# Kernel optimization log

Measured on AMD Instinct MI355X. Metric: run time of the kernel, lower is better.

The kernel has to match this reference:

```python
import jax, jax.numpy as jnp
import numpy as np

DIM = 256
HEADS = 8
HEAD_DIM = DIM // HEADS
WS = 7            # window size
SHIFT = 3         # shift size
H = 56
W = 56
B = 32
WA = WS * WS      # window area = 49
NWH, NWW = H // WS, W // WS
NW = NWH * NWW    # windows per image


def _make_attn_mask():
    # replicate the torch mask construction for the shifted windows
    img = np.zeros((H, W), dtype=np.float32)
    cnt = 0
    for hs in (slice(0, -WS), slice(-WS, -SHIFT), slice(-SHIFT, None)):
        for ws_ in (slice(0, -WS), slice(-WS, -SHIFT), slice(-SHIFT, None)):
            img[hs, ws_] = cnt
            cnt += 1
    mw = img.reshape(NWH, WS, NWW, WS).transpose(0, 2, 1, 3).reshape(-1, WA)  # (nW, 49)
    diff = mw[:, None, :] - mw[:, :, None]                                    # (nW, 49, 49)
    return np.where(diff != 0, -100.0, 0.0).astype(np.float32)


def _make_rel_index():
    coords = np.stack(np.meshgrid(np.arange(WS), np.arange(WS), indexing='ij')).reshape(2, -1)
    rel = coords[:, :, None] - coords[:, None, :]        # (2, 49, 49)
    rel = rel.transpose(1, 2, 0) + (WS - 1)              # shift to >= 0
    rel[..., 0] *= 2 * WS - 1
    return rel.sum(-1).astype(np.int32)                  # (49, 49) in [0, 169)


def setup_inputs() -> dict:
    key = jax.random.key(0)
    ks = jax.random.split(key, 12)
    s = 0.02
    inp = {
        'x': jax.random.normal(ks[0], (B, H, W, DIM), dtype=jnp.float32),
        'ln1_w': jnp.ones((DIM,), jnp.float32), 'ln1_b': jnp.zeros((DIM,), jnp.float32),
        'qkv_w': s * jax.random.normal(ks[1], (3 * DIM, DIM), jnp.float32),
        'qkv_b': jnp.zeros((3 * DIM,), jnp.float32),
        'rpb_table': s * jax.random.normal(ks[2], ((2 * WS - 1) ** 2, HEADS), jnp.float32),
        'proj_w': s * jax.random.normal(ks[3], (DIM, DIM), jnp.float32),
        'proj_b': jnp.zeros((DIM,), jnp.float32),
        'ln2_w': jnp.ones((DIM,), jnp.float32), 'ln2_b': jnp.zeros((DIM,), jnp.float32),
        'fc1_w': s * jax.random.normal(ks[4], (4 * DIM, DIM), jnp.float32),
        'fc1_b': jnp.zeros((4 * DIM,), jnp.float32),
        'ln3_w': jnp.ones((4 * DIM,), jnp.float32), 'ln3_b': jnp.zeros((4 * DIM,), jnp.float32),
        'fc2_w': s * jax.random.normal(ks[5], (DIM, 4 * DIM), jnp.float32),
        'fc2_b': jnp.zeros((DIM,), jnp.float32),
        'attn_mask': jnp.asarray(_make_attn_mask()),     # (nW, 49, 49)
        'rel_index': jnp.asarray(_make_rel_index()),     # (49, 49) int32
    }
    return inp


def _ln(x, w, b, eps=1e-5):
    m = jnp.mean(x, axis=-1, keepdims=True)
    v = jnp.mean((x - m) ** 2, axis=-1, keepdims=True)
    return (x - m) * jax.lax.rsqrt(v + eps) * w + b


def reference(x, ln1_w, ln1_b, qkv_w, qkv_b, rpb_table, proj_w, proj_b,
              ln2_w, ln2_b, fc1_w, fc1_b, ln3_w, ln3_b, fc2_w, fc2_b,
              attn_mask, rel_index):
    Bn, Hn, Wn, C = x.shape
    # ---- attention branch ----
    y = _ln(x, ln1_w, ln1_b)
    sh = jnp.roll(y, (-SHIFT, -SHIFT), axis=(1, 2))
    # window partition: (B, H, W, C) -> (B*nW, 49, C)
    win = sh.reshape(Bn, NWH, WS, NWW, WS, C).transpose(0, 1, 3, 2, 4, 5).reshape(Bn * NW, WA, C)
    qkv = win @ qkv_w.T + qkv_b                              # (Bw, 49, 3C)
    qkv = qkv.reshape(Bn * NW, WA, 3, HEADS, HEAD_DIM).transpose(2, 0, 3, 1, 4)
    q, k, v = qkv[0], qkv[1], qkv[2]                         # (Bw, h, 49, d)
    scale = HEAD_DIM ** -0.5
    attn = jnp.einsum('bhqd,bhkd->bhqk', q * scale, k)       # (Bw, h, 49, 49)
    bias = rpb_table[rel_index]                              # (49, 49, h)
    attn = attn + jnp.transpose(bias, (2, 0, 1))[None]
    attn = attn.reshape(Bn, NW, HEADS, WA, WA) + attn_mask[None, :, None]
    attn = jax.nn.softmax(attn, axis=-1).reshape(Bn * NW, HEADS, WA, WA)
    out = jnp.einsum('bhqk,bhkd->bhqd', attn, v)             # (Bw, h, 49, d)
    out = out.transpose(0, 2, 1, 3).reshape(Bn * NW, WA, C)
    out = out @ proj_w.T + proj_b
    # window reverse + un-shift
    out = out.reshape(Bn, NWH, NWW, WS, WS, C).transpose(0, 1, 3, 2, 4, 5).reshape(Bn, Hn, Wn, C)
    out = jnp.roll(out, (SHIFT, SHIFT), axis=(1, 2))
    x = x + out
    # ---- MLP branch (note: extra LayerNorm inside MLP per source) ----
    z = _ln(x, ln2_w, ln2_b)
    h = jax.nn.gelu(z @ fc1_w.T + fc1_b, approximate=False)
    h = _ln(h, ln3_w, ln3_b)
    x = x + (h @ fc2_w.T + fc2_b)
    return x
```

## Files before the change

### kernel.cpp

```cpp
#include <hip/hip_runtime.h>
#include <hip/hip_bf16.h>
#include <math.h>

typedef __attribute__((ext_vector_type(8))) short bf16x8;
typedef __attribute__((ext_vector_type(4))) float f32x4;
typedef __attribute__((ext_vector_type(4))) float f4;
typedef __attribute__((ext_vector_type(8))) unsigned short us8;
typedef __attribute__((ext_vector_type(4))) unsigned short us4;
typedef unsigned short u16;
typedef unsigned int u32;

#define HEADS 8
#define SHIFT_ 3
#define HIMG 56
#define WIMG 56
#define WA 49
#define NTOK 100352
#define NPAIR 16384

static __device__ __forceinline__ float bf2f(u16 v){ return __uint_as_float(((u32)v)<<16); }
static __device__ __forceinline__ u16 f2bf(float f){
  u32 u = __float_as_uint(f);
  return (u16)((u + 0x7fffu + ((u>>16)&1u)) >> 16);
}
static __device__ __forceinline__ u32 pkbf(float a, float b){
  __hip_bfloat162 h = __float22bfloat162_rn(make_float2(a, b));
  return *reinterpret_cast<u32*>(&h);
}
static __device__ __forceinline__ float wsum(float v){
  #pragma unroll
  for (int off=32; off>0; off>>=1) v += __shfl_xor(v, off, 64);
  return v;
}
static __device__ __forceinline__ void glds16(const u16* g, u16* l){
  __builtin_amdgcn_global_load_lds(
      (const __attribute__((address_space(1))) unsigned int*)g,
      (__attribute__((address_space(3))) unsigned int*)l, 16, 0, 0);
}
static __device__ __forceinline__ int tok2pix(int row){
  int bw = row / 49, t = row - bw*49;
  int b  = bw >> 6,  w = bw & 63;
  int wh = w >> 3,   ww = w & 7;
  int th = t / 7,    tw = t - th*7;
  int r = wh*7 + th + SHIFT_; if (r >= HIMG) r -= HIMG;
  int c = ww*7 + tw + SHIFT_; if (c >= WIMG) c -= WIMG;
  return (b*HIMG + r)*WIMG + c;
}
static __device__ __forceinline__ float gelu_f(float x){
  float e = __expf(-1.702f*x);
  return x*__builtin_amdgcn_rcpf(1.0f+e);
}

template<int C, int ISBF>
__global__ void ln_stats_kernel(const void* __restrict__ srcv, float* __restrict__ stats){
  int wave = threadIdx.x >> 6, lane = threadIdx.x & 63;
  int tok = blockIdx.x*4 + wave;
  float s=0.f, s2=0.f;
  if (ISBF == 0){
    const float* p = (const float*)srcv + (size_t)tok*C;
    #pragma unroll
    for (int i=0;i<C/256;i++){
      f4 v = *(const f4*)(p + lane*4*(C/256) + i*4);
      #pragma unroll
      for (int e=0;e<4;e++){ float f=v[e]; s+=f; s2+=f*f; }
    }
  } else {
    const u16* p = (const u16*)srcv + (size_t)tok*C;
    #pragma unroll
    for (int i=0;i<C/512;i++){
      us8 v = *(const us8*)(p + lane*8*(C/512) + i*8);
      #pragma unroll
      for (int e=0;e<8;e++){ float f=bf2f(v[e]); s+=f; s2+=f*f; }
    }
  }
  s = wsum(s); s2 = wsum(s2);
  if (lane==0){
    float mean = s/(float)C;
    float var  = s2/(float)C - mean*mean;
    stats[2*tok]   = mean;
    stats[2*tok+1] = rsqrtf(var + 1e-5f);
  }
}

__global__ void ln_apply_kernel(const float* __restrict__ src, u16* __restrict__ dst){
  int wave = threadIdx.x >> 6, lane = threadIdx.x & 63;
  int tok = blockIdx.x*4 + wave;
  const float* p = src + (size_t)tok*256;
  f4 a = *(const f4*)(p + lane*4);
  float s = a[0]+a[1]+a[2]+a[3];
  float s2 = a[0]*a[0]+a[1]*a[1]+a[2]*a[2]+a[3]*a[3];
  s = wsum(s); s2 = wsum(s2);
  float mean = s*(1.f/256.f);
  float var  = s2*(1.f/256.f) - mean*mean;
  float rstd = rsqrtf(var + 1e-5f);
  u32 o2[2];
  o2[0] = pkbf((a[0]-mean)*rstd, (a[1]-mean)*rstd);
  o2[1] = pkbf((a[2]-mean)*rstd, (a[3]-mean)*rstd);
  *(u32*)(dst + (size_t)tok*256 + lane*4)     = o2[0];
  *(u32*)(dst + (size_t)tok*256 + lane*4 + 2) = o2[1];
}

__global__ void ln_apply_b_kernel(const u16* __restrict__ src, u16* __restrict__ dst,
                                  float* __restrict__ st){
  int wave = threadIdx.x >> 6, lane = threadIdx.x & 63;
  int tok = blockIdx.x*4 + wave;
  const u16* p = src + (size_t)tok*256 + lane*4;
  us4 a4 = *(const us4*)p;
  float a0=bf2f(a4[0]), a1=bf2f(a4[1]), a2=bf2f(a4[2]), a3=bf2f(a4[3]);
  float s = a0+a1+a2+a3;
  float s2 = a0*a0+a1*a1+a2*a2+a3*a3;
  s = wsum(s); s2 = wsum(s2);
  float mean = s*(1.f/256.f);
  float var  = s2*(1.f/256.f) - mean*mean;
  float rstd = rsqrtf(var + 1e-5f);
  u32 o0 = pkbf((a0-mean)*rstd, (a1-mean)*rstd);
  u32 o1 = pkbf((a2-mean)*rstd, (a3-mean)*rstd);
  u16* d = dst + (size_t)tok*256 + lane*4;
  *(u32*)d     = o0;
  *(u32*)(d+2) = o1;
  if (lane==0){ st[2*tok] = mean; st[2*tok+1] = rstd; }
}

__global__ void prep_weights(
    const float* __restrict__ qkv_w, const float* __restrict__ qkv_b,
    const float* __restrict__ ln1w,  const float* __restrict__ ln1b,
    const float* __restrict__ fc1_w, const float* __restrict__ fc1_b,
    const float* __restrict__ ln2w,  const float* __restrict__ ln2b,
    const float* __restrict__ fc2_w, const float* __restrict__ fc2_b,
    const float* __restrict__ ln3w,  const float* __restrict__ ln3b,
    const float* __restrict__ proj_w, const float* __restrict__ proj_b,
    u16* __restrict__ wq, float* __restrict__ bq,
    u16* __restrict__ w1, float* __restrict__ b1,
    u16* __restrict__ w2, float* __restrict__ b2,
    u16* __restrict__ wp, float* __restrict__ bp,
    float* __restrict__ cs2, float* __restrict__ hstats)
{
  for (int idx = blockIdx.x*256 + threadIdx.x; idx < 2*NTOK; idx += gridDim.x*256)
    hstats[idx] = 0.f;

  int wave = threadIdx.x>>6, lane = threadIdx.x&63;
  int n = blockIdx.x*4 + wave;
  const float *W,*lw,*lb,*bs; u16* WO; float* BO; int K, row, noln, docs;
  float qs = 1.f;
  if (n < 768)      { W=qkv_w; lw=ln1w; lb=ln1b; bs=qkv_b; WO=wq; BO=bq; K=256;  row=n;      noln=0; docs=0;
                      if (n < 256) qs = 0.17677669529663689f; }
  else if (n < 1792){ W=fc1_w; lw=ln2w; lb=ln2b; bs=fc1_b; WO=w1; BO=b1; K=256;  row=n-768;  noln=0; docs=0; }
  else if (n < 2048){ W=fc2_w; lw=ln3w; lb=ln3b; bs=fc2_b; WO=w2; BO=b2; K=1024; row=n-1792; noln=0; docs=1; }
  else              { W=proj_w; lw=nullptr; lb=nullptr; bs=proj_b; WO=wp; BO=bp; K=256; row=n-2048; noln=1; docs=0; }
  float dot = 0.f, cs = 0.f;
  for (int k=lane; k<K; k+=64){
    float wv = W[(size_t)row*K + k];
    if (noln){
      WO[(size_t)row*K + k] = f2bf(wv);
    } else {
      dot += wv * lb[k];
      u16 q = f2bf(wv * lw[k] * qs);
      WO[(size_t)row*K + k] = q;
      cs += bf2f(q);
    }
  }
  dot = wsum(dot);
  if (docs){ cs = wsum(cs); if (lane==0) cs2[row] = cs; }
  if (lane==0) BO[row] = (bs[row] + dot) * qs;
}

template<int SMODE, int EPI, int SWAP, int DEPTH>
__global__ __launch_bounds__(256)
void gemm18(const void* __restrict__ Av, const u16* __restrict__ Bt,
            const float* __restrict__ stats, float* __restrict__ hstats,
            const float* __restrict__ biasf, const float* __restrict__ resid,
            const float* __restrict__ colsum, void* __restrict__ outv,
            int K, int NT, int CHUNK)
{
  constexpr int BM=128, BN=128, BK=32;
  constexpr int NBUF = DEPTH + 1;
  __shared__ u16 smem[NBUF*8192];
  constexpr int BOFF = NBUF*4096;
  int b = blockIdx.x;
  int linear = (b & 7)*CHUNK + (b >> 3);
  int mt = linear / NT, nt = linear - mt*NT;
  int m0 = mt*BM, n0 = nt*BN;
  int tid  = threadIdx.x;
  int lane = tid & 63, wave = tid >> 6;
  int wr = wave >> 1, wc = wave & 1;
  int lc16 = lane & 15, g = lane >> 4;
  int nsteps = K >> 5;

  const u16* asrc[2];
  const u16* bsrc[2];
  #pragma unroll
  for (int i=0;i<2;i++){
    int c = tid + i*256;
    int row = c >> 2, gch = ((c & 3) - (row >> 1)) & 3;
    if (SMODE <= 1){
      int grow = (SMODE==0) ? tok2pix(m0+row) : (m0+row);
      asrc[i] = (const u16*)Av + (size_t)grow*K + gch*8;
    }
    bsrc[i] = Bt + (size_t)(n0+row)*K + gch*8;
  }
  float smean[2], srstd[2];
  if (SMODE == 3){
    #pragma unroll
    for (int i=0;i<2;i++){
      int grow = m0 + ((tid + i*256) >> 2);
      smean[i] = stats[2*grow]; srstd[i] = stats[2*grow+1];
    }
  }

  f32x4 acc[4][4];
  #pragma unroll
  for (int i=0;i<4;i++)
    #pragma unroll
    for (int j=0;j<4;j++){ acc[i][j][0]=0.f; acc[i][j][1]=0.f; acc[i][j][2]=0.f; acc[i][j][3]=0.f; }

  if (SMODE <= 1){
    #pragma unroll
    for (int pt=0; pt<DEPTH; ++pt){
      int kt = pt << 5;
      #pragma unroll
      for (int i=0;i<2;i++) glds16(asrc[i]+kt, smem + pt*4096 + i*2048 + wave*512);
      #pragma unroll
      for (int i=0;i<2;i++) glds16(bsrc[i]+kt, smem + BOFF + pt*4096 + i*2048 + wave*512);
    }
    if (DEPTH == 3)      asm volatile("s_waitcnt vmcnt(8)" ::: "memory");
    else                 asm volatile("s_waitcnt vmcnt(4)" ::: "memory");
    __builtin_amdgcn_s_barrier();

    int cur = 0;
    for (int t=0; t<nsteps; ++t){
      if (t+DEPTH < nsteps){
        int ktD = (t+DEPTH) << 5;
        int nb = cur + DEPTH; if (nb >= NBUF) nb -= NBUF;
        int off = nb*4096;
        #pragma unroll
        for (int i=0;i<2;i++) glds16(asrc[i]+ktD, smem + off + i*2048 + wave*512);
        #pragma unroll
        for (int i=0;i<2;i++) glds16(bsrc[i]+ktD, smem + BOFF + off + i*2048 + wave*512);
      }
      const u16* Ap = smem + cur*4096;
      const u16* Bp = smem + BOFF + cur*4096;
      bf16x8 af[4], bfr[4];
      #pragma unroll
      for (int mi=0;mi<4;mi++){
        int r = wr*64 + mi*16 + lc16;
        u32 byte = (u32)(r*64) + ((u32)((g + (r>>1)) & 3) << 4);
        af[mi] = *(const bf16x8*)(Ap + (byte>>1));
      }
      #pragma unroll
      for (int ni=0;ni<4;ni++){
        int r = wc*64 + ni*16 + lc16;
        u32 byte = (u32)(r*64) + ((u32)((g + (r>>1)) & 3) << 4);
        bfr[ni] = *(const bf16x8*)(Bp + (byte>>1));
      }
      #pragma unroll
      for (int mi=0;mi<4;mi++)
        #pragma unroll
        for (int ni=0;ni<4;ni++)
          acc[mi][ni] = SWAP ? __builtin_amdgcn_mfma_f32_16x16x32_bf16(bfr[ni], af[mi], acc[mi][ni], 0, 0, 0)
                             : __builtin_amdgcn_mfma_f32_16x16x32_bf16(af[mi], bfr[ni], acc[mi][ni], 0, 0, 0);
      int rem = nsteps - 1 - t;
      int cnt = (rem < DEPTH) ? rem : DEPTH;
      if (cnt >= 3)      asm volatile("s_waitcnt vmcnt(8)" ::: "memory");
      else if (cnt == 2) asm volatile("s_waitcnt vmcnt(4)" ::: "memory");
      else if (cnt == 1) asm volatile("s_waitcnt vmcnt(0)" ::: "memory");
      __builtin_amdgcn_s_barrier();
      cur = (cur+1 == NBUF) ? 0 : cur+1;
    }
  } else {
    f4 rcurf[2][2];
    #pragma unroll
    for (int i=0;i<2;i++){
      int c = tid + i*256; int row = c>>2, gch = ((c&3) - (row>>1)) & 3;
      const float* ap = (const float*)Av + (size_t)(m0+row)*K + gch*8;
      rcurf[i][0] = *(const f4*)ap; rcurf[i][1] = *(const f4*)(ap+4);
    }
    for (int t=0; t<nsteps; ++t){
      int kt = t << 5;
      #pragma unroll
      for (int i=0;i<2;i++){
        int c = tid + i*256; int row = c>>2, s = c&3;
        us8 o;
        #pragma unroll
        for (int e=0;e<8;e++){
          float fv = rcurf[i][e>>2][e&3];
          o[e] = f2bf((fv - smean[i])*srstd[i]);
        }
        u32 byte = (u32)(row*64) + ((u32)s << 4);
        *(us8*)(smem + (byte>>1)) = o;
      }
      #pragma unroll
      for (int i=0;i<2;i++) glds16(bsrc[i]+kt, smem + BOFF + i*2048 + wave*512);
      __syncthreads();
      if (t+1 < nsteps){
        int kt1 = kt + 32;
        #pragma unroll
        for (int i=0;i<2;i++){
          int c = tid + i*256; int row = c>>2, gch = ((c&3) - (row>>1)) & 3;
          const float* ap = (const float*)Av + (size_t)(m0+row)*K + kt1 + gch*8;
          rcurf[i][0] = *(const f4*)ap; rcurf[i][1] = *(const f4*)(ap+4);
        }
      }
      bf16x8 af[4], bfr[4];
      #pragma unroll
      for (int mi=0;mi<4;mi++){
        int r = wr*64 + mi*16 + lc16;
        u32 byte = (u32)(r*64) + ((u32)((g + (r>>1)) & 3) << 4);
        af[mi] = *(const bf16x8*)(smem + (byte>>1));
      }
      #pragma unroll
      for (int ni=0;ni<4;ni++){
        int r = wc*64 + ni*16 + lc16;
        u32 byte = (u32)(r*64) + ((u32)((g + (r>>1)) & 3) << 4);
        bfr[ni] = *(const bf16x8*)(smem + BOFF + (byte>>1));
      }
      #pragma unroll
      for (int mi=0;mi<4;mi++)
        #pragma unroll
        for (int ni=0;ni<4;ni++)
          acc[mi][ni] = SWAP ? __builtin_amdgcn_mfma_f32_16x16x32_bf16(bfr[ni], af[mi], acc[mi][ni], 0, 0, 0)
                             : __builtin_amdgcn_mfma_f32_16x16x32_bf16(af[mi], bfr[ni], acc[mi][ni], 0, 0, 0);
      __syncthreads();
    }
  }

  int lr = lane >> 4;
  if (EPI==0){
    u16* Cs = smem;
    #pragma unroll
    for (int mi=0;mi<4;mi++){
      #pragma unroll
      for (int ni=0;ni<4;ni++){
        int cl = wc*64 + ni*16 + lc16;
        float bv = biasf[n0 + cl];
        #pragma unroll
        for (int j=0;j<4;j++){
          int rl = wr*64 + mi*16 + lr*4 + j;
          float v = acc[mi][ni][j] + bv;
          u32 byte = (u32)(rl*256 + cl*2) ^ ((u32)(rl&7)<<4);
          Cs[byte>>1] = f2bf(v);
        }
      }
    }
    __syncthreads();
    #pragma unroll
    for (int i=0;i<8;i++){
      int c = tid + i*256;
      int rl = c>>4, c0 = (c&15)*8;
      u32 byte = (u32)(rl*256 + c0*2) ^ ((u32)(rl&7)<<4);
      us8 v = *(const us8*)(Cs + (byte>>1));
      int row = m0 + rl, col = n0 + c0;
      int which = col>>8, hh = (col>>5)&7, d0 = col&31;
      int bwi = row/49, t = row - bwi*49;
      *(us8*)((u16*)outv + ((size_t)which*NPAIR + bwi*8 + hh)*(WA*32) + t*32 + d0) = v;
    }
  } else if (EPI==2){
    u16* Cs = smem;
    #pragma unroll
    for (int mi=0;mi<4;mi++){
      int rl = wr*64 + mi*16 + lc16;
      float ss = 0.f, sq = 0.f;
      #pragma unroll
      for (int ni=0;ni<4;ni++){
        int cl = wc*64 + ni*16 + g*4;
        f4 bv = *(const f4*)(biasf + n0 + cl);
        float v0 = gelu_f(acc[mi][ni][0] + bv[0]);
        float v1 = gelu_f(acc[mi][ni][1] + bv[1]);
        float v2 = gelu_f(acc[mi][ni][2] + bv[2]);
        float v3 = gelu_f(acc[mi][ni][3] + bv[3]);
        ss += (v0+v1)+(v2+v3);
        sq += (v0*v0+v1*v1)+(v2*v2+v3*v3);
        u32 w0 = pkbf(v0, v1), w1 = pkbf(v2, v3);
        u32 byte = (u32)(rl*256 + cl*2) ^ ((u32)(rl&7)<<4);
        *(u32*)(Cs + (byte>>1))     = w0;
        *(u32*)(Cs + (byte>>1) + 2) = w1;
      }
      ss += __shfl_xor(ss, 16, 64); ss += __shfl_xor(ss, 32, 64);
      sq += __shfl_xor(sq, 16, 64); sq += __shfl_xor(sq, 32, 64);
      if (g==0){
        int grow = m0 + rl;
        atomicAdd(&hstats[2*grow],   ss);
        atomicAdd(&hstats[2*grow+1], sq);
      }
    }
    __syncthreads();
    #pragma unroll
    for (int i=0;i<8;i++){
      int c = tid + i*256;
      int rl = c>>4, c0 = (c&15)*8;
      u32 byte = (u32)(rl*256 + c0*2) ^ ((u32)(rl&7)<<4);
      us8 v = *(const us8*)(Cs + (byte>>1));
      int row = m0 + rl, col = n0 + c0;
      *(us8*)((u16*)outv + (size_t)row*1024 + col) = v;
    }
  } else if (EPI==5){
    u16* Cs = smem;
    #pragma unroll
    for (int mi=0;mi<4;mi++){
      int rl = wr*64 + mi*16 + lc16;
      int pix = tok2pix(m0 + rl);
      #pragma unroll
      for (int ni=0;ni<4;ni++){
        int cl = wc*64 + ni*16 + g*4;
        int col = n0 + cl;
        f4 bv = *(const f4*)(biasf + col);
        f4 rr = *(const f4*)(resid + (size_t)pix*256 + col);
        float v0 = acc[mi][ni][0] + bv[0] + rr[0];
        float v1 = acc[mi][ni][1] + bv[1] + rr[1];
        float v2 = acc[mi][ni][2] + bv[2] + rr[2];
        float v3 = acc[mi][ni][3] + bv[3] + rr[3];
        u32 w0 = pkbf(v0, v1), w1 = pkbf(v2, v3);
        u32 byte = (u32)(rl*256 + cl*2) ^ ((u32)(rl&7)<<4);
        *(u32*)(Cs + (byte>>1))     = w0;
        *(u32*)(Cs + (byte>>1) + 2) = w1;
      }
    }
    __syncthreads();
    #pragma unroll
    for (int i=0;i<8;i++){
      int c = tid + i*256;
      int rl = c>>4, c0 = (c&15)*8;
      u32 byte = (u32)(rl*256 + c0*2) ^ ((u32)(rl&7)<<4);
      us8 v = *(const us8*)(Cs + (byte>>1));
      int pix = tok2pix(m0 + rl);
      *(us8*)((u16*)outv + (size_t)pix*256 + n0 + c0) = v;
    }
  } else {
    #pragma unroll
    for (int mi=0;mi<4;mi++){
      int rl = wr*64 + mi*16 + lc16;
      int grow = m0 + rl;
      float rs = 1.f, mr = 0.f, istd2 = 0.f, mean2 = 0.f;
      if (EPI==4 || EPI==6){
        float s = stats[2*grow], q = stats[2*grow+1];
        float mean = s*(1.f/1024.f);
        float var  = q*(1.f/1024.f) - mean*mean;
        rs = rsqrtf(var + 1e-5f);
        mr = mean*rs;
      }
      if (EPI==6){
        mean2 = hstats[2*grow];
        istd2 = __builtin_amdgcn_rcpf(hstats[2*grow+1]);
      }
      size_t rowbase = (EPI==1) ? (size_t)tok2pix(grow)*256 : (size_t)grow*256;
      #pragma unroll
      for (int ni=0;ni<4;ni++){
        int col = n0 + wc*64 + ni*16 + g*4;
        f4 bv = *(const f4*)(biasf + col);
        f4 v;
        if (EPI==4 || EPI==6){
          f4 cw = *(const f4*)(colsum + col);
          #pragma unroll
          for (int j=0;j<4;j++) v[j] = acc[mi][ni][j]*rs - mr*cw[j] + bv[j];
        } else {
          #pragma unroll
          for (int j=0;j<4;j++) v[j] = acc[mi][ni][j] + bv[j];
        }
        if (EPI==6){
          us4 xr = *(const us4*)((const u16*)resid + rowbase + col);
          #pragma unroll
          for (int j=0;j<4;j++) v[j] += bf2f(xr[j])*istd2 + mean2;
        } else {
          f4 rr = *(const f4*)(resid + rowbase + col);
          v += rr;
        }
        *(f4*)((float*)outv + rowbase + col) = v;
      }
    }
  }
}

__global__ __launch_bounds__(128)
void attn_mfma_kernel(
    const u16* __restrict__ qkv,
    const float* __restrict__ rpb,
    const int* __restrict__ rel,
    const float* __restrict__ mask,
    u16* __restrict__ outb)
{
  __shared__ u16 Kls[2][64*32];
  __shared__ u16 Vt [2][32*64];
  __shared__ u16 Pls[2][64*64];
  int wave = threadIdx.x>>6, lane = threadIdx.x&63;
  int pair = blockIdx.x*2 + wave;
  int bw = pair>>3, h = pair&7, w = bw&63;
  int lc = lane&15, g = lane>>4;
  const u16* qg = qkv + (size_t)pair*(WA*32);
  const u16* kg = qg + (size_t)NPAIR*(WA*32);
  const u16* vg = qg + (size_t)2*NPAIR*(WA*32);
  u16* Kp = &Kls[wave][0];
  u16* Vp = &Vt[wave][0];
  u16* Pp = &Pls[wave][0];

  #pragma unroll
  for (int i=0;i<4;i++){
    int idx = i*64 + lane;
    if (idx < 196) glds16(kg + idx*8, Kp + idx*8);
  }
  #pragma unroll
  for (int i=0;i<4;i++){
    int idx = i*64 + lane;
    int r = idx>>2, seg = idx&3;
    us8 vv;
    if (r < WA) vv = *(const us8*)(vg + r*32 + seg*8);
    else {
      #pragma unroll
      for (int e=0;e<8;e++) vv[e]=0;
    }
    #pragma unroll
    for (int e=0;e<8;e++){
      int d = seg*8 + e;
      u32 byte = ((u32)(d*128 + r*2)) ^ ((u32)(d&7)<<4);
      Vp[byte>>1] = vv[e];
    }
  }

  bf16x8 qa[4];
  #pragma unroll
  for (int mi=0;mi<4;mi++){
    int r = mi*16 + lc;
    if (r < WA) qa[mi] = *(const bf16x8*)(qg + r*32 + g*8);
    else { bf16x8 z;
           #pragma unroll
           for (int e=0;e<8;e++) z[e]=0; qa[mi]=z; }
  }

  f32x4 acc[4][4];
  #pragma unroll
  for (int i=0;i<4;i++)
    #pragma unroll
    for (int j=0;j<4;j++){ acc[i][j][0]=0.f; acc[i][j][1]=0.f; acc[i][j][2]=0.f; acc[i][j][3]=0.f; }

  asm volatile("s_waitcnt vmcnt(0)" ::: "memory");
  __builtin_amdgcn_s_setprio(1);
  #pragma unroll
  for (int ni=0;ni<4;ni++){
    bf16x8 kb = *(const bf16x8*)(Kp + (ni*16+lc)*32 + g*8);
    #pragma unroll
    for (int mi=0;mi<4;mi++)
      acc[mi][ni] = __builtin_amdgcn_mfma_f32_16x16x32_bf16(qa[mi], kb, acc[mi][ni], 0, 0, 0);
  }
  __builtin_amdgcn_s_setprio(0);

  float rinv[4][4];
  #pragma unroll
  for (int mi=0;mi<4;mi++){
    #pragma unroll
    for (int jr=0;jr<4;jr++){
      int i = mi*16 + g*4 + jr;
      float sv[4];
      #pragma unroll
      for (int ni=0;ni<4;ni++){
        int j = ni*16 + lc;
        float s;
        if (i < WA && j < WA){
          s = acc[mi][ni][jr] + rpb[rel[i*WA+j]*8 + h] + mask[((size_t)w*WA + i)*WA + j];
        } else s = -1e9f;
        sv[ni] = s;
      }
      float mx = fmaxf(fmaxf(sv[0],sv[1]), fmaxf(sv[2],sv[3]));
      #pragma unroll
      for (int off=1; off<16; off<<=1) mx = fmaxf(mx, __shfl_xor(mx, off, 64));
      float sum = 0.f;
      #pragma unroll
      for (int ni=0;ni<4;ni++){ sv[ni] = __expf(sv[ni]-mx); sum += sv[ni]; }
      #pragma unroll
      for (int off=1; off<16; off<<=1) sum += __shfl_xor(sum, off, 64);
      rinv[mi][jr] = __builtin_amdgcn_rcpf(sum);
      #pragma unroll
      for (int ni=0;ni<4;ni++){
        int j = ni*16 + lc;
        u32 byte = ((u32)(i*128 + j*2)) ^ ((u32)(i&7)<<4);
        Pp[byte>>1] = f2bf(sv[ni]);
      }
    }
  }

  bf16x8 vb[2][2];
  #pragma unroll
  for (int kk=0;kk<2;kk++)
    #pragma unroll
    for (int ni=0;ni<2;ni++){
      int d = ni*16 + lc;
      u32 byte = ((u32)(d*128 + kk*64 + g*16)) ^ ((u32)(d&7)<<4);
      vb[kk][ni] = *(const bf16x8*)(Vp + (byte>>1));
    }
  f32x4 aco[4][2];
  #pragma unroll
  for (int i=0;i<4;i++)
    #pragma unroll
    for (int j=0;j<2;j++){ aco[i][j][0]=0.f; aco[i][j][1]=0.f; aco[i][j][2]=0.f; aco[i][j][3]=0.f; }
  __builtin_amdgcn_s_setprio(1);
  #pragma unroll
  for (int mi=0;mi<4;mi++){
    int r = mi*16 + lc;
    #pragma unroll
    for (int kk=0;kk<2;kk++){
      u32 byte = ((u32)(r*128 + kk*64 + g*16)) ^ ((u32)(r&7)<<4);
      bf16x8 pa = *(const bf16x8*)(Pp + (byte>>1));
      #pragma unroll
      for (int ni=0;ni<2;ni++)
        aco[mi][ni] = __builtin_amdgcn_mfma_f32_16x16x32_bf16(pa, vb[kk][ni], aco[mi][ni], 0, 0, 0);
    }
  }
  __builtin_amdgcn_s_setprio(0);

  u16* Op = Kp;
  #pragma unroll
  for (int mi=0;mi<4;mi++){
    #pragma unroll
    for (int jr=0;jr<4;jr++){
      int i = mi*16 + g*4 + jr;
      if (i < WA){
        float rv = rinv[mi][jr];
        #pragma unroll
        for (int ni=0;ni<2;ni++)
          Op[i*32 + ni*16 + lc] = f2bf(aco[mi][ni][jr]*rv);
      }
    }
  }
  size_t obase = (size_t)(bw*WA)*256 + h*32;
  #pragma unroll
  for (int i=0;i<4;i++){
    int c = i*64 + lane;
    if (c < WA*4){
      int t = c>>2, seg = c&3;
      *(us8*)(outb + obase + (size_t)t*256 + seg*8) = *(const us8*)(Op + t*32 + seg*8);
    }
  }
}

extern "C" void kernel_launch(void* const* d_in, const int* in_sizes, int n_in,
                              void* d_out, int out_size, void* d_ws, size_t ws_size,
                              hipStream_t stream) {
  const float* x      = (const float*)d_in[0];
  const float* ln1w   = (const float*)d_in[1];
  const float* ln1b   = (const float*)d_in[2];
  const float* qkv_w  = (const float*)d_in[3];
  const float* qkv_b  = (const float*)d_in[4];
  const float* rpb    = (const float*)d_in[5];
  const float* proj_w = (const float*)d_in[6];
  const float* proj_b = (const float*)d_in[7];
  const float* ln2w   = (const float*)d_in[8];
  const float* ln2b   = (const float*)d_in[9];
  const float* fc1_w  = (const float*)d_in[10];
  const float* fc1_b  = (const float*)d_in[11];
  const float* ln3w   = (const float*)d_in[12];
  const float* ln3b   = (const float*)d_in[13];
  const float* fc2_w  = (const float*)d_in[14];
  const float* fc2_b  = (const float*)d_in[15];
  const float* amask  = (const float*)d_in[16];
  const int*   rel    = (const int*)d_in[17];
  float* out = (float*)d_out;

  char* ws = (char*)d_ws;
  float* hstats = (float*)(ws);
  float* stats2 = (float*)(ws +  802816);
  float* bq     = (float*)(ws + 1605632);
  float* b1     = (float*)(ws + 1608704);
  float* b2     = (float*)(ws + 1612800);
  float* bp     = (float*)(ws + 1613824);
  float* cs2    = (float*)(ws + 1614848);
  u16*   wq     = (u16*)  (ws + 1615872);
  u16*   w1     = (u16*)  (ws + 2009088);
  u16*   w2     = (u16*)  (ws + 2533376);
  u16*   wp     = (u16*)  (ws + 3057664);
  const size_t P0 = 3188736;
  u16*   qkvbuf = (u16*)(ws + P0);
  u16*   attno  = (u16*)(ws + P0 + 154140672);
  u16*   xb     = (u16*)(ws + P0 + 154140672);
  u16*   ob     = (u16*)(ws + P0);
  u16*   hbuf   = (u16*)(ws + P0);
  u16*   x1b    = (u16*)(ws + P0 + 205520896);
  const int bigws = (ws_size >= (size_t)(P0 + 205520896ull + 51380224ull));

  prep_weights<<<576,256,0,stream>>>(qkv_w,qkv_b,ln1w,ln1b, fc1_w,fc1_b,ln2w,ln2b,
                                     fc2_w,fc2_b,ln3w,ln3b, proj_w,proj_b,
                                     wq,bq, w1,b1, w2,b2, wp,bp, cs2, hstats);
  ln_apply_kernel<<<NTOK/4,256,0,stream>>>(x, xb);
  gemm18<0,0,0,2><<<784*6,256,0,stream>>>(xb, wq, nullptr, nullptr, bq, nullptr, nullptr, qkvbuf, 256, 6, 588);
  attn_mfma_kernel<<<NPAIR/2,128,0,stream>>>(qkvbuf, rpb, rel, amask, attno);
  if (bigws){
    gemm18<1,5,1,2><<<784*2,256,0,stream>>>(attno, wp, nullptr, nullptr, bp, x, nullptr, ob, 256, 2, 196);
    ln_apply_b_kernel<<<NTOK/4,256,0,stream>>>(ob, x1b, stats2);
    gemm18<1,2,1,2><<<784*8,256,0,stream>>>(x1b, w1, nullptr, hstats, b1, nullptr, nullptr, hbuf, 256, 8, 784);
    gemm18<1,6,1,2><<<784*2,256,0,stream>>>(hbuf, w2, hstats, stats2, b2, (const float*)x1b, cs2, out, 1024, 2, 196);
  } else {
    gemm18<1,1,1,2><<<784*2,256,0,stream>>>(attno, wp, nullptr, nullptr, bp, x, nullptr, out, 256, 2, 196);
    ln_stats_kernel<256,0><<<NTOK/4,256,0,stream>>>(out, stats2);
    gemm18<3,2,1,2><<<784*8,256,0,stream>>>(out, w1, stats2, hstats, b1, nullptr, nullptr, (u16*)(ws+P0), 256, 8, 784);
    gemm18<1,4,1,2><<<784*2,256,0,stream>>>((u16*)(ws+P0), w2, hstats, nullptr, b2, out, cs2, out, 1024, 2, 196);
  }
}
```

Baseline: 533.5 us.

## Precombine bias and mask into bf16 table; process two heads per wave

Adds a small pre-kernel that merges the relative-position bias gather and the shifted-window mask into one bf16 table indexed by window, head and row. The attention kernel then reads one bf16 value per score instead of an indirect rel lookup plus two float loads. Each wave now handles two (window, head) pairs, issuing the K, V and Q loads for both up front so the loads overlap. The grid is halved to match. The cost is more LDS per block, more registers for the doubled Q and V fragments, and bias plus mask rounded to bf16.

Measured after the change: 531.2 us. About the same (-0.4%).

```diff
diff --git a/kernel.cpp b/kernel.cpp
--- a/kernel.cpp
+++ b/kernel.cpp
@@ -119,6 +119,25 @@
   *(u32*)d     = o0;
   *(u32*)(d+2) = o1;
   if (lane==0){ st[2*tok] = mean; st[2*tok+1] = rstd; }
+}
+
+__global__ void cmb_kernel(const float* __restrict__ rpb, const int* __restrict__ rel,
+                           const float* __restrict__ mask, u16* __restrict__ cmb){
+  int lin = blockIdx.x*1024 + threadIdx.x*4;
+  int j0 = lin & 63;
+  int r3 = lin >> 6;
+  int i  = r3 % 49;
+  int wh = r3 / 49;
+  int h = wh & 7, w = wh >> 3;
+  us4 o;
+  #pragma unroll
+  for (int e=0;e<4;e++){
+    int j = j0 + e;
+    float v = 0.f;
+    if (j < WA) v = rpb[rel[i*WA+j]*8 + h] + mask[((size_t)w*WA + i)*WA + j];
+    o[e] = f2bf(v);
+  }
+  *(us4*)(cmb + lin) = o;
 }
 
 __global__ void prep_weights(
@@ -472,159 +491,178 @@
 __global__ __launch_bounds__(128)
 void attn_mfma_kernel(
     const u16* __restrict__ qkv,
-    const float* __restrict__ rpb,
-    const int* __restrict__ rel,
-    const float* __restrict__ mask,
+    const u16* __restrict__ cmb,
     u16* __restrict__ outb)
 {
-  __shared__ u16 Kls[2][64*32];
-  __shared__ u16 Vt [2][32*64];
-  __shared__ u16 Pls[2][64*64];
+  __shared__ u16 smem2[2][12288];
   int wave = threadIdx.x>>6, lane = threadIdx.x&63;
-  int pair = blockIdx.x*2 + wave;
-  int bw = pair>>3, h = pair&7, w = bw&63;
+  int pairbase = blockIdx.x*4 + wave*2;
+  int bw = pairbase>>3, h0 = pairbase&7, w = bw&63;
   int lc = lane&15, g = lane>>4;
-  const u16* qg = qkv + (size_t)pair*(WA*32);
-  const u16* kg = qg + (size_t)NPAIR*(WA*32);
-  const u16* vg = qg + (size_t)2*NPAIR*(WA*32);
-  u16* Kp = &Kls[wave][0];
-  u16* Vp = &Vt[wave][0];
-  u16* Pp = &Pls[wave][0];
+  u16* S = &smem2[wave][0];
+  const u16* qg0 = qkv + (size_t)pairbase*(WA*32);
+  const u16* qg1 = qg0 + WA*32;
+  const u16* kg0 = qg0 + (size_t)NPAIR*(WA*32);
+  const u16* kg1 = kg0 + WA*32;
+  const u16* vg0 = qg0 + (size_t)2*NPAIR*(WA*32);
+  const u16* vg1 = vg0 + WA*32;
 
   #pragma unroll
   for (int i=0;i<4;i++){
     int idx = i*64 + lane;
-    if (idx < 196) glds16(kg + idx*8, Kp + idx*8);
-  }
+    if (idx < 196){
+      glds16(kg0 + idx*8, S + idx*8);
+      glds16(kg1 + idx*8, S + 2048 + idx*8);
+    }
+  }
+  us8 vv0[4], vv1[4];
   #pragma unroll
   for (int i=0;i<4;i++){
-    int idx = i*64 + lane;
-    int r = idx>>2, seg = idx&3;
-    us8 vv;
-    if (r < WA) vv = *(const us8*)(vg + r*32 + seg*8);
-    else {
-      #pragma unroll
-      for (int e=0;e<8;e++) vv[e]=0;
-    }
+    int idx = i*64+lane; int r = idx>>2, seg = idx&3;
+    if (r < WA){
+      vv0[i] = *(const us8*)(vg0 + r*32 + seg*8);
+      vv1[i] = *(const us8*)(vg1 + r*32 + seg*8);
+    } else {
+      #pragma unroll
+      for (int e=0;e<8;e++){ vv0[i][e]=0; vv1[i][e]=0; }
+    }
+  }
+  bf16x8 qa0[4], qa1[4];
+  #pragma unroll
+  for (int mi=0;mi<4;mi++){
+    int r = mi*16 + lc;
+    if (r < WA){
+      qa0[mi] = *(const bf16x8*)(qg0 + r*32 + g*8);
+      qa1[mi] = *(const bf16x8*)(qg1 + r*32 + g*8);
+    } else {
+      bf16x8 z;
+      #pragma unroll
+      for (int e=0;e<8;e++) z[e]=0;
+      qa0[mi]=z; qa1[mi]=z;
+    }
+  }
+  #pragma unroll
+  for (int i=0;i<4;i++){
+    int idx = i*64+lane; int r = idx>>2, seg = idx&3;
     #pragma unroll
     for (int e=0;e<8;e++){
       int d = seg*8 + e;
       u32 byte = ((u32)(d*128 + r*2)) ^ ((u32)(d&7)<<4);
-      Vp[byte>>1] = vv[e];
-    }
-  }
-
-  bf16x8 qa[4];
-  #pragma unroll
-  for (int mi=0;mi<4;mi++){
-    int r = mi*16 + lc;
-    if (r < WA) qa[mi] = *(const bf16x8*)(qg + r*32 + g*8);
-    else { bf16x8 z;
-           #pragma unroll
-           for (int e=0;e<8;e++) z[e]=0; qa[mi]=z; }
-  }
-
-  f32x4 acc[4][4];
-  #pragma unroll
-  for (int i=0;i<4;i++)
-    #pragma unroll
-    for (int j=0;j<4;j++){ acc[i][j][0]=0.f; acc[i][j][1]=0.f; acc[i][j][2]=0.f; acc[i][j][3]=0.f; }
-
+      S[4096 + (byte>>1)] = vv0[i][e];
+      S[6144 + (byte>>1)] = vv1[i][e];
+    }
+  }
   asm volatile("s_waitcnt vmcnt(0)" ::: "memory");
-  __builtin_amdgcn_s_setprio(1);
-  #pragma unroll
-  for (int ni=0;ni<4;ni++){
-    bf16x8 kb = *(const bf16x8*)(Kp + (ni*16+lc)*32 + g*8);
-    #pragma unroll
-    for (int mi=0;mi<4;mi++)
-      acc[mi][ni] = __builtin_amdgcn_mfma_f32_16x16x32_bf16(qa[mi], kb, acc[mi][ni], 0, 0, 0);
-  }
-  __builtin_amdgcn_s_setprio(0);
-
-  float rinv[4][4];
-  #pragma unroll
-  for (int mi=0;mi<4;mi++){
-    #pragma unroll
-    for (int jr=0;jr<4;jr++){
-      int i = mi*16 + g*4 + jr;
-      float sv[4];
-      #pragma unroll
-      for (int ni=0;ni<4;ni++){
-        int j = ni*16 + lc;
-        float s;
-        if (i < WA && j < WA){
-          s = acc[mi][ni][jr] + rpb[rel[i*WA+j]*8 + h] + mask[((size_t)w*WA + i)*WA + j];
-        } else s = -1e9f;
-        sv[ni] = s;
-      }
-      float mx = fmaxf(fmaxf(sv[0],sv[1]), fmaxf(sv[2],sv[3]));
-      #pragma unroll
-      for (int off=1; off<16; off<<=1) mx = fmaxf(mx, __shfl_xor(mx, off, 64));
-      float sum = 0.f;
-      #pragma unroll
-      for (int ni=0;ni<4;ni++){ sv[ni] = __expf(sv[ni]-mx); sum += sv[ni]; }
-      #pragma unroll
-      for (int off=1; off<16; off<<=1) sum += __shfl_xor(sum, off, 64);
-      rinv[mi][jr] = __builtin_amdgcn_rcpf(sum);
-      #pragma unroll
-      for (int ni=0;ni<4;ni++){
-        int j = ni*16 + lc;
-        u32 byte = ((u32)(i*128 + j*2)) ^ ((u32)(i&7)<<4);
-        Pp[byte>>1] = f2bf(sv[ni]);
-      }
-    }
-  }
-
-  bf16x8 vb[2][2];
-  #pragma unroll
-  for (int kk=0;kk<2;kk++)
-    #pragma unroll
-    for (int ni=0;ni<2;ni++){
-      int d = ni*16 + lc;
-      u32 byte = ((u32)(d*128 + kk*64 + g*16)) ^ ((u32)(d&7)<<4);
-      vb[kk][ni] = *(const bf16x8*)(Vp + (byte>>1));
-    }
-  f32x4 aco[4][2];
-  #pragma unroll
-  for (int i=0;i<4;i++)
-    #pragma unroll
-    for (int j=0;j<2;j++){ aco[i][j][0]=0.f; aco[i][j][1]=0.f; aco[i][j][2]=0.f; aco[i][j][3]=0.f; }
-  __builtin_amdgcn_s_setprio(1);
-  #pragma unroll
-  for (int mi=0;mi<4;mi++){
-    int r = mi*16 + lc;
-    #pragma unroll
-    for (int kk=0;kk<2;kk++){
-      u32 byte = ((u32)(r*128 + kk*64 + g*16)) ^ ((u32)(r&7)<<4);
-      bf16x8 pa = *(const bf16x8*)(Pp + (byte>>1));
-      #pragma unroll
-      for (int ni=0;ni<2;ni++)
-        aco[mi][ni] = __builtin_amdgcn_mfma_f32_16x16x32_bf16(pa, vb[kk][ni], aco[mi][ni], 0, 0, 0);
-    }
-  }
-  __builtin_amdgcn_s_setprio(0);
-
-  u16* Op = Kp;
-  #pragma unroll
-  for (int mi=0;mi<4;mi++){
-    #pragma unroll
-    for (int jr=0;jr<4;jr++){
-      int i = mi*16 + g*4 + jr;
-      if (i < WA){
-        float rv = rinv[mi][jr];
+  __builtin_amdgcn_sched_barrier(0);
+
+  u16* Pp = S + 8192;
+  #pragma unroll
+  for (int p=0; p<2; ++p){
+    const u16* Kp = S + p*2048;
+    const u16* Vp = S + 4096 + p*2048;
+    const u16* cmbp = cmb + ((size_t)((w*8 + h0 + p)*49))*64;
+
+    f32x4 acc[4][4];
+    #pragma unroll
+    for (int i=0;i<4;i++)
+      #pragma unroll
+      for (int j=0;j<4;j++){ acc[i][j][0]=0.f; acc[i][j][1]=0.f; acc[i][j][2]=0.f; acc[i][j][3]=0.f; }
+
+    __builtin_amdgcn_s_setprio(1);
+    #pragma unroll
+    for (int ni=0;ni<4;ni++){
+      bf16x8 kb = *(const bf16x8*)(Kp + (ni*16+lc)*32 + g*8);
+      #pragma unroll
+      for (int mi=0;mi<4;mi++)
+        acc[mi][ni] = __builtin_amdgcn_mfma_f32_16x16x32_bf16(p==0 ? qa0[mi] : qa1[mi], kb, acc[mi][ni], 0, 0, 0);
+    }
+    __builtin_amdgcn_s_setprio(0);
+
+    float rinv[4][4];
+    #pragma unroll
+    for (int mi=0;mi<4;mi++){
+      #pragma unroll
+      for (int jr=0;jr<4;jr++){
+        int i = mi*16 + g*4 + jr;
+        float sv[4];
+        #pragma unroll
+        for (int ni=0;ni<4;ni++){
+          int j = ni*16 + lc;
+          float s;
+          if (i < WA && j < WA){
+            s = acc[mi][ni][jr] + bf2f(cmbp[i*64 + j]);
+          } else s = -1e9f;
+          sv[ni] = s;
+        }
+        float mx = fmaxf(fmaxf(sv[0],sv[1]), fmaxf(sv[2],sv[3]));
+        #pragma unroll
+        for (int off=1; off<16; off<<=1) mx = fmaxf(mx, __shfl_xor(mx, off, 64));
+        float sum = 0.f;
+        #pragma unroll
+        for (int ni=0;ni<4;ni++){ sv[ni] = __expf(sv[ni]-mx); sum += sv[ni]; }
+        #pragma unroll
+        for (int off=1; off<16; off<<=1) sum += __shfl_xor(sum, off, 64);
+        rinv[mi][jr] = __builtin_amdgcn_rcpf(sum);
+        #pragma unroll
+        for (int ni=0;ni<4;ni++){
+          int j = ni*16 + lc;
+          u32 byte = ((u32)(i*128 + j*2)) ^ ((u32)(i&7)<<4);
+          Pp[byte>>1] = f2bf(sv[ni]);
+        }
+      }
+    }
+
+    bf16x8 vb[2][2];
+    #pragma unroll
+    for (int kk=0;kk<2;kk++)
+      #pragma unroll
+      for (int ni=0;ni<2;ni++){
+        int d = ni*16 + lc;
+        u32 byte = ((u32)(d*128 + kk*64 + g*16)) ^ ((u32)(d&7)<<4);
+        vb[kk][ni] = *(const bf16x8*)(Vp + (byte>>1));
+      }
+    f32x4 aco[4][2];
+    #pragma unroll
+    for (int i=0;i<4;i++)
+      #pragma unroll
+      for (int j=0;j<2;j++){ aco[i][j][0]=0.f; aco[i][j][1]=0.f; aco[i][j][2]=0.f; aco[i][j][3]=0.f; }
+    __builtin_amdgcn_s_setprio(1);
+    #pragma unroll
+    for (int mi=0;mi<4;mi++){
+      int r = mi*16 + lc;
+      #pragma unroll
+      for (int kk=0;kk<2;kk++){
+        u32 byte = ((u32)(r*128 + kk*64 + g*16)) ^ ((u32)(r&7)<<4);
+        bf16x8 pa = *(const bf16x8*)(Pp + (byte>>1));
         #pragma unroll
         for (int ni=0;ni<2;ni++)
-          Op[i*32 + ni*16 + lc] = f2bf(aco[mi][ni][jr]*rv);
-      }
-    }
-  }
-  size_t obase = (size_t)(bw*WA)*256 + h*32;
-  #pragma unroll
-  for (int i=0;i<4;i++){
-    int c = i*64 + lane;
-    if (c < WA*4){
-      int t = c>>2, seg = c&3;
-      *(us8*)(outb + obase + (size_t)t*256 + seg*8) = *(const us8*)(Op + t*32 + seg*8);
+          aco[mi][ni] = __builtin_amdgcn_mfma_f32_16x16x32_bf16(pa, vb[kk][ni], aco[mi][ni], 0, 0, 0);
+      }
+    }
+    __builtin_amdgcn_s_setprio(0);
+
+    u16* Op = S + p*2048;
+    #pragma unroll
+    for (int mi=0;mi<4;mi++){
+      #pragma unroll
+      for (int jr=0;jr<4;jr++){
+        int i = mi*16 + g*4 + jr;
+        if (i < WA){
+          float rv = rinv[mi][jr];
+          #pragma unroll
+          for (int ni=0;ni<2;ni++)
+            Op[i*32 + ni*16 + lc] = f2bf(aco[mi][ni][jr]*rv);
+        }
+      }
+    }
+    size_t obase = (size_t)(bw*WA)*256 + (h0+p)*32;
+    #pragma unroll
+    for (int i=0;i<4;i++){
+      int c = i*64 + lane;
+      if (c < WA*4){
+        int t = c>>2, seg = c&3;
+        *(us8*)(outb + obase + (size_t)t*256 + seg*8) = *(const us8*)(Op + t*32 + seg*8);
+      }
     }
   }
 }
@@ -671,14 +709,16 @@
   u16*   ob     = (u16*)(ws + P0);
   u16*   hbuf   = (u16*)(ws + P0);
   u16*   x1b    = (u16*)(ws + P0 + 205520896);
+  u16*   cmb    = (u16*)(ws + P0 + 205520896);
   const int bigws = (ws_size >= (size_t)(P0 + 205520896ull + 51380224ull));
 
   prep_weights<<<576,256,0,stream>>>(qkv_w,qkv_b,ln1w,ln1b, fc1_w,fc1_b,ln2w,ln2b,
                                      fc2_w,fc2_b,ln3w,ln3b, proj_w,proj_b,
                                      wq,bq, w1,b1, w2,b2, wp,bp, cs2, hstats);
+  cmb_kernel<<<1568,256,0,stream>>>(rpb, rel, amask, cmb);
   ln_apply_kernel<<<NTOK/4,256,0,stream>>>(x, xb);
   gemm18<0,0,0,2><<<784*6,256,0,stream>>>(xb, wq, nullptr, nullptr, bq, nullptr, nullptr, qkvbuf, 256, 6, 588);
-  attn_mfma_kernel<<<NPAIR/2,128,0,stream>>>(qkvbuf, rpb, rel, amask, attno);
+  attn_mfma_kernel<<<NPAIR/4,128,0,stream>>>(qkvbuf, cmb, attno);
   if (bigws){
     gemm18<1,5,1,2><<<784*2,256,0,stream>>>(attno, wp, nullptr, nullptr, bp, x, nullptr, ob, 256, 2, 196);
     ln_apply_b_kernel<<<NTOK/4,256,0,stream>>>(ob, x1b, stats2);
```
